# Performance work log

Hardware: AMD Instinct MI355X
Metric: run time of the kernel (lower is better)

The kernel has to match this reference:

```python
import jax, jax.numpy as jnp
import numpy as np
import math

DIM = 1024
H = 16          # num_heads
DH = 64         # dim_head
FD = 32         # feature_dim = int(0.5 * dim_head)
B = 4
S = 4096
EPS = 1e-8


def setup_inputs() -> dict:
    key = jax.random.key(0)
    ks = jax.random.split(key, 10)
    inner = H * DH
    x = jax.random.normal(ks[0], (B, S, DIM), dtype=jnp.float32)
    # Linear weights stored as [in, out] (transposed torch layout), small init scale
    Wq = jax.random.normal(ks[1], (DIM, inner), dtype=jnp.float32) * 0.02
    bq = jnp.zeros((inner,), dtype=jnp.float32)
    Wk = jax.random.normal(ks[2], (DIM, inner), dtype=jnp.float32) * 0.02
    bk = jnp.zeros((inner,), dtype=jnp.float32)
    Wv = jax.random.normal(ks[3], (DIM, inner), dtype=jnp.float32) * 0.02
    bv = jnp.zeros((inner,), dtype=jnp.float32)
    Wo = jax.random.normal(ks[4], (inner, DIM), dtype=jnp.float32) * 0.02
    bo = jnp.zeros((DIM,), dtype=jnp.float32)
    # proj_matrix buffer: QR of randn(dim_head, feature_dim), scaled by sqrt(dim_head)
    rm = np.asarray(jax.random.normal(ks[5], (DH, FD), dtype=jnp.float32))
    q_orth, _ = np.linalg.qr(rm)
    proj = jnp.asarray(q_orth, dtype=jnp.float32) * math.sqrt(DH)
    return {"x": x, "Wq": Wq, "bq": bq, "Wk": Wk, "bk": bk,
            "Wv": Wv, "bv": bv, "proj": proj, "Wo": Wo, "bo": bo}


def _heads(t, b, n):
    # [b, n, H*DH] -> [b, H, n, DH]
    return t.reshape(b, n, H, DH).transpose(0, 2, 1, 3)


def reference(x, Wq, bq, Wk, bk, Wv, bv, proj, Wo, bo):
    b, n, _ = x.shape
    q = _heads(x @ Wq + bq, b, n)   # bhnd
    k = _heads(x @ Wk + bk, b, n)
    v = _heads(x @ Wv + bv, b, n)
    inv_sqrt_f = 1.0 / math.sqrt(FD)
    q_prime = jax.nn.relu(jnp.einsum('bhnd,df->bhnf', q, proj)) * inv_sqrt_f
    k_prime = jax.nn.relu(jnp.einsum('bhnd,df->bhnf', k, proj)) * inv_sqrt_f
    kv = jnp.einsum('bhnf,bhnd->bhfd', k_prime, v)          # [b,h,FD,DH]
    z = 1.0 / (jnp.einsum('bhnf,bhf->bhn', q_prime, k_prime.sum(axis=2)) + EPS)
    attn = jnp.einsum('bhnf,bhfd->bhnd', q_prime, kv) * z[..., None]
    attn = attn.transpose(0, 2, 1, 3).reshape(b, n, H * DH)
    return attn @ Wo + bo            # dropout in eval mode = identity
```

## Files before the change

### kernel.cpp

```cpp
#include <hip/hip_runtime.h>

typedef unsigned short u16;
typedef __attribute__((ext_vector_type(8))) short bf16x8;
typedef __attribute__((ext_vector_type(4))) float f32x4;

__device__ inline float bf2f(u16 u) {
    unsigned v = ((unsigned)u) << 16;
    return __builtin_bit_cast(float, v);
}
__device__ inline u16 f2bf(float f) {
    unsigned u = __builtin_bit_cast(unsigned, f);
    u += 0x7fff + ((u >> 16) & 1);
    return (u16)(u >> 16);
}

__device__ inline void gload_lds16(const void* g, void* l) {
    __builtin_amdgcn_global_load_lds(
        (const __attribute__((address_space(1))) unsigned int*)(unsigned long long)g,
        (__attribute__((address_space(3))) unsigned int*)(unsigned)(unsigned long long)l,
        16, 0, 0);
}

__global__ __launch_bounds__(256) void cast_x(const float4* __restrict__ x,
                                              bf16x8* __restrict__ xb) {
    long i = (long)blockIdx.x * 256 + threadIdx.x;
    float4 v0 = x[2 * i];
    float4 v1 = x[2 * i + 1];
    bf16x8 o;
    o[0] = (short)f2bf(v0.x); o[1] = (short)f2bf(v0.y);
    o[2] = (short)f2bf(v0.z); o[3] = (short)f2bf(v0.w);
    o[4] = (short)f2bf(v1.x); o[5] = (short)f2bf(v1.y);
    o[6] = (short)f2bf(v1.z); o[7] = (short)f2bf(v1.w);
    xb[i] = o;
}

__global__ __launch_bounds__(256) void fold_qk(
    const float* __restrict__ Wq, const float* __restrict__ Wk,
    const float* __restrict__ bq, const float* __restrict__ bk,
    const float* __restrict__ proj,
    u16* __restrict__ WallT, float* __restrict__ bias_all)
{
    const int bid = blockIdx.x;
    const int tid = threadIdx.x;
    const int qk = bid >> 7, h = (bid >> 3) & 15, kt = bid & 7;
    const float* W  = qk ? Wk : Wq;
    const float* bb = qk ? bk : bq;
    const int kin0 = kt * 128;
    __shared__ float pj[64 * 32];
    __shared__ float panel[128 * 64];
    {
        const float4* ps = (const float4*)proj;
        float4* pd = (float4*)pj;
        #pragma unroll
        for (int it = 0; it < 2; ++it) pd[it * 256 + tid] = ps[it * 256 + tid];
    }
    #pragma unroll
    for (int it = 0; it < 8; ++it) {
        const int li = it * 256 + tid;
        const int row = li >> 4, c4 = (li & 15) * 4;
        *(float4*)&panel[row * 64 + c4] =
            *(const float4*)&W[(long)(kin0 + row) * 1024 + h * 64 + c4];
    }
    __syncthreads();

    const int f = tid & 31, g = tid >> 5;
    float pjr[64];
    #pragma unroll
    for (int d = 0; d < 64; ++d) pjr[d] = pj[d * 32 + f];

    alignas(16) u16 outv[16];
    #pragma unroll
    for (int rr = 0; rr < 16; ++rr) {
        const float4* prow = (const float4*)&panel[(g * 16 + rr) * 64];
        float acc = 0.f;
        #pragma unroll
        for (int d4 = 0; d4 < 16; ++d4) {
            float4 p = prow[d4];
            acc += p.x * pjr[d4 * 4]     + p.y * pjr[d4 * 4 + 1]
                 + p.z * pjr[d4 * 4 + 2] + p.w * pjr[d4 * 4 + 3];
        }
        outv[rr] = f2bf(acc);
    }
    u16* dst = WallT + (long)(qk * 512 + h * 32 + f) * 1024 + kin0 + g * 16;
    *(bf16x8*)dst     = *(const bf16x8*)&outv[0];
    *(bf16x8*)&dst[8] = *(const bf16x8*)&outv[8];

    if (kt == 0 && g == 0) {
        float a = 0.f;
        #pragma unroll
        for (int d = 0; d < 64; ++d) a += bb[h * 64 + d] * pjr[d];
        bias_all[qk * 512 + h * 32 + f] = a;
    }
}

__global__ __launch_bounds__(256) void transpose_vo(
    const float* __restrict__ Wv, const float* __restrict__ Wo,
    const float* __restrict__ bv,
    u16* __restrict__ WallT, u16* __restrict__ WoT, float* __restrict__ bias_all)
{
    const int bid = blockIdx.x;
    const int tid = threadIdx.x;
    const bool isV = (bid < 256);
    const int tile = isV ? bid : (bid - 256);
    const int kt = tile >> 4, ct = tile & 15;
    const float* src = isV ? Wv : Wo;
    __shared__ float T[64][65];
    #pragma unroll
    for (int it = 0; it < 16; ++it) {
        const int kl = it * 4 + (tid >> 6);
        T[kl][tid & 63] = src[(long)(kt * 64 + kl) * 1024 + ct * 64 + (tid & 63)];
    }
    __syncthreads();
    #pragma unroll
    for (int it = 0; it < 2; ++it) {
        const int li = it * 256 + tid;
        const int cl = li >> 3, k8 = (li & 7) * 8;
        bf16x8 o;
        #pragma unroll
        for (int j = 0; j < 8; ++j) o[j] = (short)f2bf(T[k8 + j][cl]);
        u16* dst = isV ? (WallT + (long)(1024 + ct * 64 + cl) * 1024)
                       : (WoT   + (long)(ct * 64 + cl) * 1024);
        *(bf16x8*)&dst[kt * 64 + k8] = o;
    }
    if (isV && kt == 0 && tid < 64) bias_all[1024 + ct * 64 + tid] = bv[ct * 64 + tid];
}

template<int NBN, bool RELUQK, typename OutT>
__global__ __launch_bounds__(512, 2) void gemm256(
    const u16* __restrict__ A, const u16* __restrict__ Bt,
    const float* __restrict__ bias, OutT* __restrict__ C)
{
    constexpr int NWG   = 64 * NBN;
    constexpr int NCOLS = NBN * 256;
    __shared__ alignas(16) u16 lds[65536];

    const int bid = blockIdx.x;
    const int wg  = (bid & 7) * (NWG / 8) + (bid >> 3);
    const long m0 = (long)(wg / NBN) * 256;
    const long n0 = (long)(wg % NBN) * 256;

    const int tid  = threadIdx.x;
    const int wave = tid >> 6, lane = tid & 63;
    const int wm = wave >> 2, wn = wave & 3;

    const int srow = wave * 32 + (lane >> 2);
    const int gch  = ((lane & 3) ^ ((lane >> 3) & 3)) * 8;
    const u16* pA0 = A  + (m0 + srow) * 1024 + gch;
    const u16* pA1 = pA0 + 16 * 1024;
    const u16* pB0 = Bt + (n0 + srow) * 1024 + gch;
    const u16* pB1 = pB0 + 16 * 1024;

    #define SUB(b_,kh_,ab_) (lds + (((b_)*2+(kh_))*2+(ab_))*8192)
    #define STG_A(b_,kh_,t_) { const int k0_ = (t_)*64 + (kh_)*32;            \
        u16* d_ = SUB(b_,kh_,0) + wave * 1024;                                \
        gload_lds16(pA0 + k0_, d_); gload_lds16(pA1 + k0_, d_ + 512); }
    #define STG_B(b_,kh_,t_) { const int k0_ = (t_)*64 + (kh_)*32;            \
        u16* d_ = SUB(b_,kh_,1) + wave * 1024;                                \
        gload_lds16(pB0 + k0_, d_); gload_lds16(pB1 + k0_, d_ + 512); }

    const int m  = lane & 15, kc = lane >> 4;
    const int off  = (kc ^ ((m >> 1) & 3)) * 8;
    const int arow = (wm * 128 + m) * 32 + off;
    const int brow = (wn * 64  + m) * 32 + off;

    f32x4  acc[8][4] = {};
    bf16x8 af[8];
    bf16x8 b0, b1;

    #define DSA(b_,kh_) { const u16* s_ = SUB(b_,kh_,0);                      \
        _Pragma("unroll") for (int mt_ = 0; mt_ < 8; ++mt_)                   \
            af[mt_] = *(const bf16x8*)(s_ + arow + mt_ * 512); }
    #define DSB(b_,kh_,nh_) { const u16* s_ = SUB(b_,kh_,1) + brow + (nh_)*1024; \
        b0 = *(const bf16x8*)(s_); b1 = *(const bf16x8*)(s_ + 512); }
    #define MM(nh_) { _Pragma("unroll") for (int mt_ = 0; mt_ < 8; ++mt_) {   \
        acc[mt_][(nh_)*2]   = __builtin_amdgcn_mfma_f32_16x16x32_bf16(        \
            af[mt_], b0, acc[mt_][(nh_)*2],   0, 0, 0);                       \
        acc[mt_][(nh_)*2+1] = __builtin_amdgcn_mfma_f32_16x16x32_bf16(        \
            af[mt_], b1, acc[mt_][(nh_)*2+1], 0, 0, 0); } }
    #define BARMM(nh_)                                                        \
        __builtin_amdgcn_s_barrier();                                         \
        asm volatile("s_waitcnt lgkmcnt(0)" ::: "memory");                    \
        __builtin_amdgcn_s_setprio(1);                                        \
        MM(nh_);                                                              \
        __builtin_amdgcn_s_setprio(0);                                        \
        __builtin_amdgcn_s_barrier();

    STG_A(0,0,0); STG_B(0,0,0);
    STG_A(0,1,0); STG_B(0,1,0);
    STG_A(1,0,1); STG_B(1,0,1);
    asm volatile("s_waitcnt vmcnt(4)" ::: "memory");
    __builtin_amdgcn_s_barrier();

    #pragma unroll 1
    for (int i = 0; i < 8; ++i) {
        const int  t1   = 2 * i + 1;
        const bool more = (i < 7);
        DSA(0,0); DSB(0,0,0);
        STG_A(1,1,t1);
        BARMM(0);
        DSB(0,0,1);
        STG_B(1,1,t1);
        BARMM(1);
        DSA(0,1); DSB(0,1,0);
        if (more) STG_A(0,0,t1+1);
        BARMM(0);
        DSB(0,1,1);
        if (more) {
            STG_B(0,0,t1+1);
            asm volatile("s_waitcnt vmcnt(4)" ::: "memory");
        } else {
            asm volatile("s_waitcnt vmcnt(0)" ::: "memory");
        }
        BARMM(1);
        DSA(1,0); DSB(1,0,0);
        if (more) STG_A(0,1,t1+1);
        BARMM(0);
        DSB(1,0,1);
        if (more) STG_B(0,1,t1+1);
        BARMM(1);
        DSA(1,1); DSB(1,1,0);
        if (more) STG_A(1,0,t1+2);
        BARMM(0);
        DSB(1,1,1);
        if (more) {
            STG_B(1,0,t1+2);
            asm volatile("s_waitcnt vmcnt(4)" ::: "memory");
        }
        BARMM(1);
    }

    if constexpr (sizeof(OutT) == 2) {
        const bool dorelu = RELUQK && (n0 < 1024);
        #pragma unroll
        for (int nf = 0; nf < 4; ++nf) {
            const int col = wn * 64 + nf * 16 + m;
            const float bval = bias[n0 + col];
            #pragma unroll
            for (int mt = 0; mt < 8; ++mt) {
                #pragma unroll
                for (int r = 0; r < 4; ++r) {
                    const int row = wm * 128 + mt * 16 + kc * 4 + r;
                    float c = acc[mt][nf][r] + bval;
                    if (dorelu) c = fmaxf(c, 0.f) * 0.17677669529663687f;
                    const int x = ((row >> 2) & 7) << 1;
                    lds[row * 256 + (((col >> 3) ^ x) << 3) + (col & 7)] = f2bf(c);
                }
            }
        }
        __syncthreads();
        #pragma unroll
        for (int it = 0; it < 16; ++it) {
            const int li = it * 512 + tid;
            const int row = li >> 5, ch = li & 31;
            const int x = ((row >> 2) & 7) << 1;
            bf16x8 v = *(const bf16x8*)&lds[row * 256 + ((ch ^ x) << 3)];
            *(bf16x8*)&C[(m0 + row) * (long)NCOLS + n0 + ch * 8] = v;
        }
    } else {
        float* ft = (float*)lds;
        #pragma unroll 1
        for (int half = 0; half < 2; ++half) {
            __syncthreads();
            if (wm == half) {
                #pragma unroll
                for (int nf = 0; nf < 4; ++nf) {
                    const int col = wn * 64 + nf * 16 + m;
                    const float bval = bias[n0 + col];
                    #pragma unroll
                    for (int mt = 0; mt < 8; ++mt) {
                        #pragma unroll
                        for (int r = 0; r < 4; ++r) {
                            const int row = mt * 16 + kc * 4 + r;
                            const int x = ((row >> 2) & 7) << 1;
                            ft[row * 256 + (((col >> 2) ^ x) << 2) + (col & 3)] =
                                acc[mt][nf][r] + bval;
                        }
                    }
                }
            }
            __syncthreads();
            #pragma unroll
            for (int it = 0; it < 16; ++it) {
                const int li = it * 512 + tid;
                const int row = li >> 6, ch = li & 63;
                const int x = ((row >> 2) & 7) << 1;
                float4 v = *(const float4*)&ft[row * 256 + ((ch ^ x) << 2)];
                *(float4*)&C[(m0 + half * 128 + row) * (long)NCOLS + n0 + ch * 4] = v;
            }
        }
    }
    #undef SUB
    #undef STG_A
    #undef STG_B
    #undef DSA
    #undef DSB
    #undef MM
    #undef BARMM
}

__global__ __launch_bounds__(256) void kv_v3(const u16* __restrict__ Y,
                                             float* __restrict__ part_kv,
                                             float* __restrict__ part_ks)
{
    __shared__ float ksf[128 * 33];
    __shared__ float vsf[128 * 68];
    const int bh = blockIdx.x, c = blockIdx.y;
    const int b = bh >> 4, h = bh & 15;
    const int tid = threadIdx.x;
    const long rbase = (long)b * 4096 + (long)c * 128;

    #pragma unroll
    for (int it = 0; it < 2; ++it) {
        const int lr = it * 64 + (tid >> 2), cc = (tid & 3) * 8;
        bf16x8 kx = *(const bf16x8*)(Y + (rbase + lr) * 2048 + 512 + h * 32 + cc);
        #pragma unroll
        for (int j = 0; j < 8; ++j) ksf[lr * 33 + cc + j] = bf2f((u16)kx[j]);
    }
    #pragma unroll
    for (int it = 0; it < 4; ++it) {
        const int lr = it * 32 + (tid >> 3), cc = (tid & 7) * 8;
        bf16x8 vx = *(const bf16x8*)(Y + (rbase + lr) * 2048 + 1024 + h * 64 + cc);
        #pragma unroll
        for (int j = 0; j < 8; ++j) vsf[lr * 68 + cc + j] = bf2f((u16)vx[j]);
    }
    __syncthreads();

    const int f = tid >> 3, dg = (tid & 7) * 8;
    float acc[8] = {};
    float ksacc = 0.f;
    #pragma unroll 4
    for (int n = 0; n < 128; ++n) {
        const float kf = ksf[n * 33 + f];
        const float4 v0 = *(const float4*)&vsf[n * 68 + dg];
        const float4 v1 = *(const float4*)&vsf[n * 68 + dg + 4];
        acc[0] += kf * v0.x; acc[1] += kf * v0.y;
        acc[2] += kf * v0.z; acc[3] += kf * v0.w;
        acc[4] += kf * v1.x; acc[5] += kf * v1.y;
        acc[6] += kf * v1.z; acc[7] += kf * v1.w;
        ksacc += kf;
    }

    float* o = part_kv + (((long)bh * 32 + c) * 32 + f) * 64 + dg;
    *(f32x4*)o       = f32x4{acc[0], acc[1], acc[2], acc[3]};
    *(f32x4*)(o + 4) = f32x4{acc[4], acc[5], acc[6], acc[7]};
    if ((tid & 7) == 0) part_ks[(bh * 32 + c) * 32 + f] = ksacc;
}

__global__ __launch_bounds__(256) void kv_reduce(const float* __restrict__ part_kv,
                                                 const float* __restrict__ part_ks,
                                                 float* __restrict__ kv,
                                                 float* __restrict__ ksum)
{
    const int idx = blockIdx.x * 256 + threadIdx.x;
    if (blockIdx.x < 512) {
        const int bh = idx >> 11, off = idx & 2047;
        const float* p = part_kv + (long)bh * 65536 + off;
        float s = 0.f;
        #pragma unroll 8
        for (int c = 0; c < 32; c++) s += p[c * 2048];
        kv[idx] = s;
    } else {
        const int i2 = idx - 512 * 256;
        const int bh = i2 >> 5, f = i2 & 31;
        const float* p = part_ks + bh * 1024 + f;
        float s = 0.f;
        #pragma unroll 8
        for (int c = 0; c < 32; c++) s += p[c * 32];
        ksum[i2] = s;
    }
}

__global__ __launch_bounds__(256) void attn_v2(const u16* __restrict__ Y,
                                               const float* __restrict__ kv,
                                               const float* __restrict__ ksum,
                                               u16* __restrict__ attn)
{
    __shared__ float qsf[64 * 36];
    __shared__ float kss[32];
    __shared__ float zs[64];
    const int tid = threadIdx.x;
    const int bh = blockIdx.x;
    const int b = bh >> 4, h = bh & 15;
    const long row0 = (long)b * 4096 + (long)blockIdx.y * 64;

    {
        const int lr = tid >> 2, c8 = (tid & 3) * 8;
        bf16x8 qx = *(const bf16x8*)(Y + (row0 + lr) * 2048 + h * 32 + c8);
        #pragma unroll
        for (int j = 0; j < 8; ++j) qsf[lr * 36 + c8 + j] = bf2f((u16)qx[j]);
    }
    if (tid < 32) kss[tid] = ksum[bh * 32 + tid];

    const int wave = tid >> 6, lane = tid & 63;
    const float* kvg = kv + (long)bh * 2048 + lane;
    float kvreg[32];
    #pragma unroll
    for (int ff = 0; ff < 32; ++ff) kvreg[ff] = kvg[ff * 64];

    __syncthreads();

    {
        const int lr = wave * 16 + (lane & 15);
        float den = 0.f;
        #pragma unroll
        for (int fc = 0; fc < 8; ++fc) {
            const float4 q = *(const float4*)&qsf[lr * 36 + fc * 4];
            den += q.x * kss[fc * 4]     + q.y * kss[fc * 4 + 1]
                 + q.z * kss[fc * 4 + 2] + q.w * kss[fc * 4 + 3];
        }
        if (lane < 16) zs[lr] = 1.f / (den + 1e-8f);
    }
    __syncthreads();

    #pragma unroll
    for (int rg = 0; rg < 4; ++rg) {
        const int lr0 = wave * 16 + rg * 4;
        float acc0 = 0.f, acc1 = 0.f, acc2 = 0.f, acc3 = 0.f;
        #pragma unroll
        for (int fc = 0; fc < 8; ++fc) {
            const float4 q0 = *(const float4*)&qsf[(lr0 + 0) * 36 + fc * 4];
            const float4 q1 = *(const float4*)&qsf[(lr0 + 1) * 36 + fc * 4];
            const float4 q2 = *(const float4*)&qsf[(lr0 + 2) * 36 + fc * 4];
            const float4 q3 = *(const float4*)&qsf[(lr0 + 3) * 36 + fc * 4];
            const float k0 = kvreg[fc * 4], k1 = kvreg[fc * 4 + 1];
            const float k2 = kvreg[fc * 4 + 2], k3 = kvreg[fc * 4 + 3];
            acc0 += q0.x * k0 + q0.y * k1 + q0.z * k2 + q0.w * k3;
            acc1 += q1.x * k0 + q1.y * k1 + q1.z * k2 + q1.w * k3;
            acc2 += q2.x * k0 + q2.y * k1 + q2.z * k2 + q2.w * k3;
            acc3 += q3.x * k0 + q3.y * k1 + q3.z * k2 + q3.w * k3;
        }
        u16* op = attn + (row0 + lr0) * 1024 + h * 64 + lane;
        op[0]        = f2bf(acc0 * zs[lr0 + 0]);
        op[1024]     = f2bf(acc1 * zs[lr0 + 1]);
        op[2 * 1024] = f2bf(acc2 * zs[lr0 + 2]);
        op[3 * 1024] = f2bf(acc3 * zs[lr0 + 3]);
    }
}

extern "C" void kernel_launch(void* const* d_in, const int* in_sizes, int n_in,
                              void* d_out, int out_size, void* d_ws, size_t ws_size,
                              hipStream_t stream)
{
    const float* x    = (const float*)d_in[0];
    const float* Wq   = (const float*)d_in[1];
    const float* bq   = (const float*)d_in[2];
    const float* Wk   = (const float*)d_in[3];
    const float* bk   = (const float*)d_in[4];
    const float* Wv   = (const float*)d_in[5];
    const float* bv   = (const float*)d_in[6];
    const float* proj = (const float*)d_in[7];
    const float* Wo   = (const float*)d_in[8];
    const float* bo   = (const float*)d_in[9];

    char* w = (char*)d_ws;
    u16*   xbf     = (u16*)  (w);
    float* part_kv = (float*)(w);
    u16*   attn    = (u16*)  (w);
    u16*   wallT   = (u16*)  (w + 33554432);
    u16*   woT     = (u16*)  (w + 37748736);
    float* bias    = (float*)(w + 39845888);
    float* kv      = (float*)(w + 39854080);
    float* ksum    = (float*)(w + 40378368);
    u16*   Y       = (u16*)  (w + 40386560);
    float* part_ks = (float*)(w + 107495424);

    cast_x<<<8192, 256, 0, stream>>>((const float4*)x, (bf16x8*)xbf);

    fold_qk<<<256, 256, 0, stream>>>(Wq, Wk, bq, bk, proj, wallT, bias);

    transpose_vo<<<512, 256, 0, stream>>>(Wv, Wo, bv, wallT, woT, bias);

    gemm256<8, true, u16><<<512, 512, 0, stream>>>(xbf, wallT, bias, Y);

    kv_v3<<<dim3(64, 32), 256, 0, stream>>>(Y, part_kv, part_ks);

    kv_reduce<<<520, 256, 0, stream>>>(part_kv, part_ks, kv, ksum);

    attn_v2<<<dim3(64, 64), 256, 0, stream>>>(Y, kv, ksum, attn);

    gemm256<4, false, float><<<256, 512, 0, stream>>>(attn, woT, bo, (float*)d_out);
}
```

Before: 318.5 us.

## Merge prep kernels into one launch and split QKV GEMM into two launches

The cast, Q/K fold and V/O transpose kernels are merged into a single prep kernel that picks its role from the block index, removing two launches and the idle gaps between them. The first projection GEMM is split into two launches of 256 workgroups, each covering half the rows through a new row-offset parameter, and the block swizzle now uses gridDim. The split adds a launch and gives each launch less parallel work, possibly to better fit one wave of workgroups on the device.

```diff
diff --git a/kernel.cpp b/kernel.cpp
--- a/kernel.cpp
+++ b/kernel.cpp
@@ -21,122 +21,119 @@
         16, 0, 0);
 }
 
-__global__ __launch_bounds__(256) void cast_x(const float4* __restrict__ x,
-                                              bf16x8* __restrict__ xb) {
-    long i = (long)blockIdx.x * 256 + threadIdx.x;
-    float4 v0 = x[2 * i];
-    float4 v1 = x[2 * i + 1];
-    bf16x8 o;
-    o[0] = (short)f2bf(v0.x); o[1] = (short)f2bf(v0.y);
-    o[2] = (short)f2bf(v0.z); o[3] = (short)f2bf(v0.w);
-    o[4] = (short)f2bf(v1.x); o[5] = (short)f2bf(v1.y);
-    o[6] = (short)f2bf(v1.z); o[7] = (short)f2bf(v1.w);
-    xb[i] = o;
-}
-
-__global__ __launch_bounds__(256) void fold_qk(
+__global__ __launch_bounds__(256) void prep(
+    const float4* __restrict__ x, bf16x8* __restrict__ xb,
     const float* __restrict__ Wq, const float* __restrict__ Wk,
     const float* __restrict__ bq, const float* __restrict__ bk,
     const float* __restrict__ proj,
-    u16* __restrict__ WallT, float* __restrict__ bias_all)
-{
-    const int bid = blockIdx.x;
-    const int tid = threadIdx.x;
-    const int qk = bid >> 7, h = (bid >> 3) & 15, kt = bid & 7;
-    const float* W  = qk ? Wk : Wq;
-    const float* bb = qk ? bk : bq;
-    const int kin0 = kt * 128;
-    __shared__ float pj[64 * 32];
-    __shared__ float panel[128 * 64];
-    {
-        const float4* ps = (const float4*)proj;
-        float4* pd = (float4*)pj;
-        #pragma unroll
-        for (int it = 0; it < 2; ++it) pd[it * 256 + tid] = ps[it * 256 + tid];
-    }
-    #pragma unroll
-    for (int it = 0; it < 8; ++it) {
-        const int li = it * 256 + tid;
-        const int row = li >> 4, c4 = (li & 15) * 4;
-        *(float4*)&panel[row * 64 + c4] =
-            *(const float4*)&W[(long)(kin0 + row) * 1024 + h * 64 + c4];
-    }
-    __syncthreads();
-
-    const int f = tid & 31, g = tid >> 5;
-    float pjr[64];
-    #pragma unroll
-    for (int d = 0; d < 64; ++d) pjr[d] = pj[d * 32 + f];
-
-    alignas(16) u16 outv[16];
-    #pragma unroll
-    for (int rr = 0; rr < 16; ++rr) {
-        const float4* prow = (const float4*)&panel[(g * 16 + rr) * 64];
-        float acc = 0.f;
-        #pragma unroll
-        for (int d4 = 0; d4 < 16; ++d4) {
-            float4 p = prow[d4];
-            acc += p.x * pjr[d4 * 4]     + p.y * pjr[d4 * 4 + 1]
-                 + p.z * pjr[d4 * 4 + 2] + p.w * pjr[d4 * 4 + 3];
-        }
-        outv[rr] = f2bf(acc);
-    }
-    u16* dst = WallT + (long)(qk * 512 + h * 32 + f) * 1024 + kin0 + g * 16;
-    *(bf16x8*)dst     = *(const bf16x8*)&outv[0];
-    *(bf16x8*)&dst[8] = *(const bf16x8*)&outv[8];
-
-    if (kt == 0 && g == 0) {
-        float a = 0.f;
-        #pragma unroll
-        for (int d = 0; d < 64; ++d) a += bb[h * 64 + d] * pjr[d];
-        bias_all[qk * 512 + h * 32 + f] = a;
-    }
-}
-
-__global__ __launch_bounds__(256) void transpose_vo(
     const float* __restrict__ Wv, const float* __restrict__ Wo,
     const float* __restrict__ bv,
     u16* __restrict__ WallT, u16* __restrict__ WoT, float* __restrict__ bias_all)
 {
+    __shared__ float smem[10240];
     const int bid = blockIdx.x;
     const int tid = threadIdx.x;
-    const bool isV = (bid < 256);
-    const int tile = isV ? bid : (bid - 256);
-    const int kt = tile >> 4, ct = tile & 15;
-    const float* src = isV ? Wv : Wo;
-    __shared__ float T[64][65];
-    #pragma unroll
-    for (int it = 0; it < 16; ++it) {
-        const int kl = it * 4 + (tid >> 6);
-        T[kl][tid & 63] = src[(long)(kt * 64 + kl) * 1024 + ct * 64 + (tid & 63)];
-    }
-    __syncthreads();
-    #pragma unroll
-    for (int it = 0; it < 2; ++it) {
-        const int li = it * 256 + tid;
-        const int cl = li >> 3, k8 = (li & 7) * 8;
+
+    if (bid < 8192) {
+        long i = (long)bid * 256 + tid;
+        float4 v0 = x[2 * i];
+        float4 v1 = x[2 * i + 1];
         bf16x8 o;
-        #pragma unroll
-        for (int j = 0; j < 8; ++j) o[j] = (short)f2bf(T[k8 + j][cl]);
-        u16* dst = isV ? (WallT + (long)(1024 + ct * 64 + cl) * 1024)
-                       : (WoT   + (long)(ct * 64 + cl) * 1024);
-        *(bf16x8*)&dst[kt * 64 + k8] = o;
-    }
-    if (isV && kt == 0 && tid < 64) bias_all[1024 + ct * 64 + tid] = bv[ct * 64 + tid];
+        o[0] = (short)f2bf(v0.x); o[1] = (short)f2bf(v0.y);
+        o[2] = (short)f2bf(v0.z); o[3] = (short)f2bf(v0.w);
+        o[4] = (short)f2bf(v1.x); o[5] = (short)f2bf(v1.y);
+        o[6] = (short)f2bf(v1.z); o[7] = (short)f2bf(v1.w);
+        xb[i] = o;
+    } else if (bid < 8448) {
+        const int fb = bid - 8192;
+        const int qk = fb >> 7, h = (fb >> 3) & 15, kt = fb & 7;
+        const float* W  = qk ? Wk : Wq;
+        const float* bb = qk ? bk : bq;
+        const int kin0 = kt * 128;
+        float* pj    = smem;
+        float* panel = smem + 2048;
+        {
+            const float4* ps = (const float4*)proj;
+            float4* pd = (float4*)pj;
+            #pragma unroll
+            for (int it = 0; it < 2; ++it) pd[it * 256 + tid] = ps[it * 256 + tid];
+        }
+        #pragma unroll
+        for (int it = 0; it < 8; ++it) {
+            const int li = it * 256 + tid;
+            const int row = li >> 4, c4 = (li & 15) * 4;
+            *(float4*)&panel[row * 64 + c4] =
+                *(const float4*)&W[(long)(kin0 + row) * 1024 + h * 64 + c4];
+        }
+        __syncthreads();
+
+        const int f = tid & 31, g = tid >> 5;
+        float pjr[64];
+        #pragma unroll
+        for (int d = 0; d < 64; ++d) pjr[d] = pj[d * 32 + f];
+
+        alignas(16) u16 outv[16];
+        #pragma unroll
+        for (int rr = 0; rr < 16; ++rr) {
+            const float4* prow = (const float4*)&panel[(g * 16 + rr) * 64];
+            float acc = 0.f;
+            #pragma unroll
+            for (int d4 = 0; d4 < 16; ++d4) {
+                float4 p = prow[d4];
+                acc += p.x * pjr[d4 * 4]     + p.y * pjr[d4 * 4 + 1]
+                     + p.z * pjr[d4 * 4 + 2] + p.w * pjr[d4 * 4 + 3];
+            }
+            outv[rr] = f2bf(acc);
+        }
+        u16* dst = WallT + (long)(qk * 512 + h * 32 + f) * 1024 + kin0 + g * 16;
+        *(bf16x8*)dst     = *(const bf16x8*)&outv[0];
+        *(bf16x8*)&dst[8] = *(const bf16x8*)&outv[8];
+
+        if (kt == 0 && g == 0) {
+            float a = 0.f;
+            #pragma unroll
+            for (int d = 0; d < 64; ++d) a += bb[h * 64 + d] * pjr[d];
+            bias_all[qk * 512 + h * 32 + f] = a;
+        }
+    } else {
+        const int tb = bid - 8448;
+        const bool isV = (tb < 256);
+        const int tile = isV ? tb : (tb - 256);
+        const int kt = tile >> 4, ct = tile & 15;
+        const float* src = isV ? Wv : Wo;
+        float* T = smem;
+        #pragma unroll
+        for (int it = 0; it < 16; ++it) {
+            const int kl = it * 4 + (tid >> 6);
+            T[kl * 65 + (tid & 63)] = src[(long)(kt * 64 + kl) * 1024 + ct * 64 + (tid & 63)];
+        }
+        __syncthreads();
+        #pragma unroll
+        for (int it = 0; it < 2; ++it) {
+            const int li = it * 256 + tid;
+            const int cl = li >> 3, k8 = (li & 7) * 8;
+            bf16x8 o;
+            #pragma unroll
+            for (int j = 0; j < 8; ++j) o[j] = (short)f2bf(T[(k8 + j) * 65 + cl]);
+            u16* dst = isV ? (WallT + (long)(1024 + ct * 64 + cl) * 1024)
+                           : (WoT   + (long)(ct * 64 + cl) * 1024);
+            *(bf16x8*)&dst[kt * 64 + k8] = o;
+        }
+        if (isV && kt == 0 && tid < 64) bias_all[1024 + ct * 64 + tid] = bv[ct * 64 + tid];
+    }
 }
 
 template<int NBN, bool RELUQK, typename OutT>
 __global__ __launch_bounds__(512, 2) void gemm256(
     const u16* __restrict__ A, const u16* __restrict__ Bt,
-    const float* __restrict__ bias, OutT* __restrict__ C)
-{
-    constexpr int NWG   = 64 * NBN;
+    const float* __restrict__ bias, OutT* __restrict__ C, long moff)
+{
     constexpr int NCOLS = NBN * 256;
     __shared__ alignas(16) u16 lds[65536];
 
     const int bid = blockIdx.x;
-    const int wg  = (bid & 7) * (NWG / 8) + (bid >> 3);
-    const long m0 = (long)(wg / NBN) * 256;
+    const int wg  = (bid & 7) * ((int)gridDim.x >> 3) + (bid >> 3);
+    const long m0 = moff + (long)(wg / NBN) * 256;
     const long n0 = (long)(wg % NBN) * 256;
 
     const int tid  = threadIdx.x;
@@ -464,13 +461,12 @@
     u16*   Y       = (u16*)  (w + 40386560);
     float* part_ks = (float*)(w + 107495424);
 
-    cast_x<<<8192, 256, 0, stream>>>((const float4*)x, (bf16x8*)xbf);
-
-    fold_qk<<<256, 256, 0, stream>>>(Wq, Wk, bq, bk, proj, wallT, bias);
-
-    transpose_vo<<<512, 256, 0, stream>>>(Wv, Wo, bv, wallT, woT, bias);
-
-    gemm256<8, true, u16><<<512, 512, 0, stream>>>(xbf, wallT, bias, Y);
+    prep<<<8960, 256, 0, stream>>>((const float4*)x, (bf16x8*)xbf,
+                                   Wq, Wk, bq, bk, proj, Wv, Wo, bv,
+                                   wallT, woT, bias);
+
+    gemm256<8, true, u16><<<256, 512, 0, stream>>>(xbf, wallT, bias, Y, 0L);
+    gemm256<8, true, u16><<<256, 512, 0, stream>>>(xbf, wallT, bias, Y, 8192L);
 
     kv_v3<<<dim3(64, 32), 256, 0, stream>>>(Y, part_kv, part_ks);
 
@@ -478,5 +474,5 @@
 
     attn_v2<<<dim3(64, 64), 256, 0, stream>>>(Y, kv, ksum, attn);
 
-    gemm256<4, false, float><<<256, 512, 0, stream>>>(attn, woT, bo, (float*)d_out);
-}
+    gemm256<4, false, float><<<256, 512, 0, stream>>>(attn, woT, bo, (float*)d_out, 0L);
+}
```

Result: no change. 315.6 us (-0.9%).
